# Kernel optimization log

Measured on AMD Instinct MI355X. Metric: run time of the kernel, lower is better.

## Reference

```python
import jax, jax.numpy as jnp
import numpy as np

BETA = 0.25  # commitment loss weight (module default beta=0.25)
K = 1024     # num_of_embeddings


def setup_inputs() -> dict:
    key = jax.random.key(0)
    k1, k2 = jax.random.split(key)
    inputs = jax.random.normal(k1, (16, 256, 64, 64), dtype=jnp.float32)  # NCHW
    codebook = jax.random.normal(k2, (K, 256), dtype=jnp.float32)         # [K, D]
    return {"inputs": inputs, "codebook": codebook}


def reference(inputs, codebook):
    # NCHW -> NHWC, flatten to [N, D]
    x = jnp.transpose(inputs, (0, 2, 3, 1))
    shape_nhwc = x.shape
    flat = x.reshape(-1, codebook.shape[1])  # [N, D]

    dist = (jnp.sum(flat * flat, axis=1, keepdims=True)
            + jnp.sum(codebook * codebook, axis=1)
            - 2.0 * flat @ codebook.T)  # [N, K]
    idx = jnp.argmin(dist, axis=1)  # [N]

    # one-hot @ codebook is just a gather
    zq = codebook[idx].reshape(shape_nhwc)  # [B, H, W, D]

    commitment_loss = jnp.mean((zq - x) ** 2)
    loss = BETA * commitment_loss

    # straight-through estimator
    zq_st = x + jax.lax.stop_gradient(zq - x)

    # perplexity: avg one-hot probs == normalized histogram of code usage
    n = flat.shape[0]
    counts = jnp.zeros((K,), dtype=flat.dtype).at[idx].add(1.0)
    avg_probs = counts / n
    perplexity = jnp.exp(-jnp.sum(avg_probs * jnp.log(avg_probs + 1e-10)))

    z_out = jnp.transpose(zq_st, (0, 3, 1, 2))  # back to NCHW
    return z_out, loss, perplexity, idx[:, None]
```

## Files before the change

### kernel.cpp

```cpp
#include <hip/hip_runtime.h>
#include <math.h>

#define NPTS   65536
#define DDIM   256
#define KCODES 1024
#define HWSZ   4096
#define ZELEMS 16777216
#define CHW    1048576


typedef __attribute__((ext_vector_type(8))) short s16x8;
typedef __attribute__((ext_vector_type(4))) float f32x4;

#define AS1 __attribute__((address_space(1)))
#define AS3 __attribute__((address_space(3)))

__device__ __forceinline__ void bf16split(float x, unsigned short& h, unsigned short& l) {
    unsigned u  = __float_as_uint(x);
    unsigned hu = (u + 0x8000u) & 0xFFFF0000u;
    h = (unsigned short)(hu >> 16);
    float r = x - __uint_as_float(hu);
    l = (unsigned short)((__float_as_uint(r) + 0x8000u) >> 16);
}

__global__ __launch_bounds__(256) void conv_w(const float* __restrict__ cb,
                                              unsigned short* __restrict__ Ws,
                                              float* __restrict__ ww) {
    int gid  = blockIdx.x * 256 + threadIdx.x;
    int code = gid >> 3, o32 = gid & 7;
    int ct = code >> 8, r256 = code & 255, rh = r256 >> 7, rr = r256 & 127;
    unsigned short hi[32], lo[32];
    float ss = 0.f;
#pragma unroll
    for (int j4 = 0; j4 < 8; ++j4) {
        float4 v = *(const float4*)(cb + (size_t)code * DDIM + o32 * 32 + j4 * 4);
        ss += v.x * v.x + v.y * v.y + v.z * v.z + v.w * v.w;
        bf16split(v.x, hi[j4*4+0], lo[j4*4+0]);
        bf16split(v.y, hi[j4*4+1], lo[j4*4+1]);
        bf16split(v.z, hi[j4*4+2], lo[j4*4+2]);
        bf16split(v.w, hi[j4*4+3], lo[j4*4+3]);
    }
    ss += __shfl_down(ss, 4, 8);
    ss += __shfl_down(ss, 2, 8);
    ss += __shfl_down(ss, 1, 8);
    if (o32 == 0) ww[code] = ss;
    size_t bh = (size_t)ct * 131072 + (size_t)o32       * 8192 + rh * 4096 + (rr >> 4) * 512;
    size_t bl = (size_t)ct * 131072 + (size_t)(o32 + 8) * 8192 + rh * 4096 + (rr >> 4) * 512;
#pragma unroll
    for (int oct = 0; oct < 4; ++oct) {
        size_t fo = (size_t)((rr & 15) + 16 * oct) * 8;
        *(s16x8*)(Ws + bh + fo) = *(const s16x8*)&hi[oct * 8];
        *(s16x8*)(Ws + bl + fo) = *(const s16x8*)&lo[oct * 8];
    }
}

__global__ __launch_bounds__(256) void conv_x(const float* __restrict__ in,
                                              unsigned short* __restrict__ Xs,
                                              float* __restrict__ xxpart) {
    __shared__ float xt[32 * 128];
    __shared__ float xps[4];
    const int tid = threadIdx.x;
    const int rg = blockIdx.x >> 3, dc = blockIdx.x & 7;
    const int mt = rg >> 1, rhalf = rg & 1;
    const int b = (rg * 128) >> 12, hw0 = (rg * 128) & 4095;
    const float* src = in + (size_t)b * CHW + (size_t)(dc * 32) * HWSZ + hw0;
    float xs = 0.f;
#pragma unroll
    for (int r = 0; r < 16; ++r) {
        int e = r * 256 + tid, dd = e >> 7, i = e & 127;
        float v = src[(size_t)dd * HWSZ + i];
        xt[dd * 128 + i] = v;
        xs += v * v;
    }
#pragma unroll
    for (int o = 32; o; o >>= 1) xs += __shfl_down(xs, o, 64);
    if ((tid & 63) == 0) xps[tid >> 6] = xs;
    __syncthreads();
    if (tid == 0) xxpart[blockIdx.x] = xps[0] + xps[1] + xps[2] + xps[3];
#pragma unroll
    for (int hl = 0; hl < 2; ++hl) {
        int g = hl * 256 + tid;
        int row = g >> 2, o = g & 3;
        unsigned short hi[8], lo[8];
#pragma unroll
        for (int j = 0; j < 8; ++j)
            bf16split(xt[(o * 8 + j) * 128 + row], hi[j], lo[j]);
        size_t fo = rhalf * 4096 + (size_t)(row >> 4) * 512 + (size_t)((row & 15) + 16 * o) * 8;
        size_t bh = (size_t)mt * 131072 + (size_t)dc       * 8192 + fo;
        size_t bl = (size_t)mt * 131072 + (size_t)(dc + 8) * 8192 + fo;
        *(s16x8*)(Xs + bh) = *(const s16x8*)hi;
        *(s16x8*)(Xs + bl) = *(const s16x8*)lo;
    }
}

__global__ __launch_bounds__(512) void gemm_argmin(
        const unsigned short* __restrict__ Xs, const unsigned short* __restrict__ Ws,
        const float* __restrict__ ww, unsigned long long* __restrict__ pbest) {
    __shared__ unsigned short lds[24576];
    const int tid = threadIdx.x, lane = tid & 63, w = tid >> 6;
    const int wm = w >> 2, wn = w & 3;
    const int col = lane & 15, q = lane >> 4;
    const int bid = blockIdx.x;
    const int xcd = bid & 7, slot = bid >> 3;
    const int nt = slot & 3, mb = (slot >> 2) * 8 + xcd;

    const unsigned short* XsB = Xs + (size_t)mb * 131072;
    const unsigned short* WsB = Ws + (size_t)nt * 131072
                              + (wn >> 1) * 4096 + (wn & 1) * 2048 + lane * 8;

    f32x4 acc[8][4] = {};
    s16x8 B0[4], B1[4];
    const int aoff = wm * 4096 + lane * 8;

    auto SA = [&](int g, int p) {
        const int kA = (g & 7) | ((g >> 4) << 3);
        const unsigned short* s0 = XsB + kA * 8192 + tid * 8;
        __builtin_amdgcn_global_load_lds((const AS1 unsigned*)s0,
            (AS3 unsigned*)&lds[p * 8192 + w * 512], 16, 0, 0);
        __builtin_amdgcn_global_load_lds((const AS1 unsigned*)(s0 + 4096),
            (AS3 unsigned*)&lds[p * 8192 + 4096 + w * 512], 16, 0, 0);
    };
    auto LB = [&](int g, s16x8* B) {
        const int kW = (g & 7) | (((g >> 3) & 1) << 3);
        const s16x8* src = (const s16x8*)(WsB + kW * 8192);
        B[0] = src[0]; B[1] = src[64]; B[2] = src[128]; B[3] = src[192];
    };
#define BAR do { __builtin_amdgcn_s_barrier(); __builtin_amdgcn_sched_barrier(0); } while (0)

    auto TILE = [&](int g, int p, int pstg, const s16x8* Bc, s16x8* Bn, int gate) {
        s16x8 a[8];
#pragma unroll
        for (int mf = 0; mf < 8; ++mf)
            a[mf] = *(const s16x8*)&lds[p * 8192 + aoff + mf * 512];
        if (g + 1 < 24) LB(g + 1, Bn);
        if (g + 2 < 24) SA(g + 2, pstg);
        if (gate == 6)      asm volatile("s_waitcnt vmcnt(6)" ::: "memory");
        else if (gate == 4) asm volatile("s_waitcnt vmcnt(4)" ::: "memory");
        else                asm volatile("s_waitcnt vmcnt(0)" ::: "memory");
        __builtin_amdgcn_sched_barrier(0);
        __builtin_amdgcn_s_setprio(1);
#pragma unroll
        for (int mf = 0; mf < 8; ++mf) {
            acc[mf][0] = __builtin_amdgcn_mfma_f32_16x16x32_bf16(a[mf], Bc[0], acc[mf][0], 0, 0, 0);
            acc[mf][1] = __builtin_amdgcn_mfma_f32_16x16x32_bf16(a[mf], Bc[1], acc[mf][1], 0, 0, 0);
            acc[mf][2] = __builtin_amdgcn_mfma_f32_16x16x32_bf16(a[mf], Bc[2], acc[mf][2], 0, 0, 0);
            acc[mf][3] = __builtin_amdgcn_mfma_f32_16x16x32_bf16(a[mf], Bc[3], acc[mf][3], 0, 0, 0);
        }
        __builtin_amdgcn_s_setprio(0);
        BAR;
    };

    SA(0, 0);
    LB(0, B0);
    SA(1, 1);
    asm volatile("s_waitcnt vmcnt(2)" ::: "memory");
    BAR;

    for (int t6 = 0; t6 < 3; ++t6) {
        TILE(t6 * 6 + 0, 0, 2, B0, B1, 6);
        TILE(t6 * 6 + 1, 1, 0, B1, B0, 6);
        TILE(t6 * 6 + 2, 2, 1, B0, B1, 6);
        TILE(t6 * 6 + 3, 0, 2, B1, B0, 6);
        TILE(t6 * 6 + 4, 1, 0, B0, B1, 6);
        TILE(t6 * 6 + 5, 2, 1, B1, B0, 6);
    }
    TILE(18, 0, 2, B0, B1, 6);
    TILE(19, 1, 0, B1, B0, 6);
    TILE(20, 2, 1, B0, B1, 6);
    TILE(21, 0, 2, B1, B0, 6);
    TILE(22, 1, 0, B0, B1, 4);
    TILE(23, 2, 1, B1, B0, 0);

    __syncthreads();
    unsigned long long* kbuf = (unsigned long long*)lds;
    float wv[4];
#pragma unroll
    for (int nf = 0; nf < 4; ++nf) wv[nf] = ww[nt * 256 + wn * 64 + nf * 16 + col];
#pragma unroll
    for (int mf = 0; mf < 8; ++mf)
#pragma unroll
        for (int r = 0; r < 4; ++r) {
            unsigned long long key = ~0ull;
#pragma unroll
            for (int nf = 0; nf < 4; ++nf) {
                int kg = nt * 256 + wn * 64 + nf * 16 + col;
                float sd = wv[nf] - 2.f * acc[mf][nf][r];
                unsigned u = __float_as_uint(sd);
                u = (u & 0x80000000u) ? ~u : (u | 0x80000000u);
                unsigned long long kk = ((unsigned long long)u << 32) | (unsigned)kg;
                key = kk < key ? kk : key;
            }
#pragma unroll
            for (int off = 1; off < 4; off <<= 1) {
                unsigned klo = __shfl_xor((unsigned)key, off, 64);
                unsigned khi = __shfl_xor((unsigned)(key >> 32), off, 64);
                unsigned long long ok = ((unsigned long long)khi << 32) | klo;
                key = ok < key ? ok : key;
            }
            if ((col & 3) == 0)
                kbuf[(wm * 128 + mf * 16 + q * 4 + r) * 17 + wn * 4 + (col >> 2)] = key;
        }
    __syncthreads();
    if (tid < 256) {
        const unsigned long long* rowp = kbuf + tid * 17;
        unsigned long long km = rowp[0];
#pragma unroll
        for (int i = 1; i < 16; ++i) {
            unsigned long long k = rowp[i];
            km = k < km ? k : km;
        }
        pbest[(size_t)nt * 65536 + mb * 256 + tid] = km;
    }
#undef BAR
}

__global__ __launch_bounds__(256) void gather_kernel(
        const float* __restrict__ cb, const unsigned long long* __restrict__ pbest,
        float* __restrict__ idx_out, unsigned int* __restrict__ counts,
        float* __restrict__ zout, float* __restrict__ partials) {
    const int tid = threadIdx.x;
    const int n   = blockIdx.x * 256 + tid;
    unsigned long long km = pbest[n];
#pragma unroll
    for (int nt = 1; nt < 4; ++nt) {
        unsigned long long k = pbest[(size_t)nt * 65536 + n];
        km = k < km ? k : km;
    }
    const int r = (int)(km & 0xFFFFFFFFu);
    idx_out[n] = (float)r;
    atomicAdd(&counts[r], 1u);

    unsigned m = (unsigned)(km >> 32);
    m = (m & 0x80000000u) ? (m & 0x7FFFFFFFu) : ~m;
    float sd = __uint_as_float(m);

    const int b = n >> 12, hw = n & 4095;
    const float4* row4 = (const float4*)(cb + (size_t)r * DDIM);
    float* zp = zout + (size_t)b * CHW + hw;
#pragma unroll 8
    for (int c4 = 0; c4 < 64; ++c4) {
        float4 v = row4[c4];
        zp[(size_t)(c4 * 4 + 0) * HWSZ] = v.x;
        zp[(size_t)(c4 * 4 + 1) * HWSZ] = v.y;
        zp[(size_t)(c4 * 4 + 2) * HWSZ] = v.z;
        zp[(size_t)(c4 * 4 + 3) * HWSZ] = v.w;
    }
#pragma unroll
    for (int o = 32; o; o >>= 1) sd += __shfl_down(sd, o, 64);
    __shared__ float ps[4];
    if ((tid & 63) == 0) ps[tid >> 6] = sd;
    __syncthreads();
    if (tid == 0) partials[blockIdx.x] = ps[0] + ps[1] + ps[2] + ps[3];
}

__global__ __launch_bounds__(256) void final_kernel(
        const float* __restrict__ partials, const float* __restrict__ xxpart,
        const unsigned int* __restrict__ counts,
        float* __restrict__ out_loss, float* __restrict__ out_perp) {
    const int tid = threadIdx.x;
    float s = partials[tid];
#pragma unroll
    for (int i = 0; i < 16; ++i) s += xxpart[tid * 16 + i];
    float e = 0.f;
#pragma unroll
    for (int qq = 0; qq < 4; ++qq) {
        float p = (float)counts[tid * 4 + qq] * (1.f / 65536.f);
        e += p * logf(p + 1e-10f);
    }
#pragma unroll
    for (int o = 32; o; o >>= 1) {
        s += __shfl_down(s, o, 64);
        e += __shfl_down(e, o, 64);
    }
    __shared__ float ss[4], es[4];
    if ((tid & 63) == 0) { ss[tid >> 6] = s; es[tid >> 6] = e; }
    __syncthreads();
    if (tid == 0) {
        float S = ss[0] + ss[1] + ss[2] + ss[3];
        float E = es[0] + es[1] + es[2] + es[3];
        *out_loss = 0.25f * (S / (float)ZELEMS);
        *out_perp = expf(-E);
    }
}

extern "C" void kernel_launch(void* const* d_in, const int* in_sizes, int n_in,
                              void* d_out, int out_size, void* d_ws, size_t ws_size,
                              hipStream_t stream) {
    (void)in_sizes; (void)n_in; (void)out_size; (void)ws_size;
    const float* in = (const float*)d_in[0];
    const float* cb = (const float*)d_in[1];
    float* out  = (float*)d_out;
    float* zout = out;
    float* loss = out + ZELEMS;
    float* perp = out + ZELEMS + 1;
    float* idxf = out + ZELEMS + 2;

    unsigned int*       counts   = (unsigned int*)d_ws;
    float*              ww       = (float*)((char*)d_ws + 4096);
    float*              partials = (float*)((char*)d_ws + 8192);
    unsigned short*     Ws       = (unsigned short*)((char*)d_ws + 16384);
    unsigned long long* pbest    = (unsigned long long*)((char*)d_ws + 1064960);
    float*              xxpart   = (float*)((char*)d_ws + 3162112);
    unsigned short*     Xs       = (unsigned short*)zout;

    hipMemsetAsync(counts, 0, 4096, stream);
    conv_w      <<<32,   256, 0, stream>>>(cb, Ws, ww);
    conv_x      <<<4096, 256, 0, stream>>>(in, Xs, xxpart);
    gemm_argmin <<<1024, 512, 0, stream>>>(Xs, Ws, ww, pbest);
    gather_kernel<<<256, 256, 0, stream>>>(cb, pbest, idxf, counts, zout, partials);
    final_kernel <<<1,   256, 0, stream>>>(partials, xxpart, counts, loss, perp);
}
```

Baseline: 189.5 us.

## Deepen LDS pipeline to six stages and barrier every other tile

```diff
diff --git a/kernel.cpp b/kernel.cpp
--- a/kernel.cpp
+++ b/kernel.cpp
@@ -96,7 +96,7 @@
 __global__ __launch_bounds__(512) void gemm_argmin(
         const unsigned short* __restrict__ Xs, const unsigned short* __restrict__ Ws,
         const float* __restrict__ ww, unsigned long long* __restrict__ pbest) {
-    __shared__ unsigned short lds[24576];
+    __shared__ unsigned short lds[49152];
     const int tid = threadIdx.x, lane = tid & 63, w = tid >> 6;
     const int wm = w >> 2, wn = w & 3;
     const int col = lane & 15, q = lane >> 4;
@@ -127,13 +127,14 @@
     };
 #define BAR do { __builtin_amdgcn_s_barrier(); __builtin_amdgcn_sched_barrier(0); } while (0)
 
-    auto TILE = [&](int g, int p, int pstg, const s16x8* Bc, s16x8* Bn, int gate) {
+    auto TILE = [&](int g, int p, int pstg, const s16x8* Bc, s16x8* Bn,
+                    int gate, bool dobar) {
         s16x8 a[8];
 #pragma unroll
         for (int mf = 0; mf < 8; ++mf)
             a[mf] = *(const s16x8*)&lds[p * 8192 + aoff + mf * 512];
         if (g + 1 < 24) LB(g + 1, Bn);
-        if (g + 2 < 24) SA(g + 2, pstg);
+        if (g + 4 < 24) SA(g + 4, pstg);
         if (gate == 6)      asm volatile("s_waitcnt vmcnt(6)" ::: "memory");
         else if (gate == 4) asm volatile("s_waitcnt vmcnt(4)" ::: "memory");
         else                asm volatile("s_waitcnt vmcnt(0)" ::: "memory");
@@ -147,29 +148,28 @@
             acc[mf][3] = __builtin_amdgcn_mfma_f32_16x16x32_bf16(a[mf], Bc[3], acc[mf][3], 0, 0, 0);
         }
         __builtin_amdgcn_s_setprio(0);
-        BAR;
+        if (dobar) BAR;
     };
 
-    SA(0, 0);
+    SA(0, 0); SA(1, 1); SA(2, 2); SA(3, 3);
     LB(0, B0);
-    SA(1, 1);
-    asm volatile("s_waitcnt vmcnt(2)" ::: "memory");
+    asm volatile("s_waitcnt vmcnt(4)" ::: "memory");
     BAR;
 
     for (int t6 = 0; t6 < 3; ++t6) {
-        TILE(t6 * 6 + 0, 0, 2, B0, B1, 6);
-        TILE(t6 * 6 + 1, 1, 0, B1, B0, 6);
-        TILE(t6 * 6 + 2, 2, 1, B0, B1, 6);
-        TILE(t6 * 6 + 3, 0, 2, B1, B0, 6);
-        TILE(t6 * 6 + 4, 1, 0, B0, B1, 6);
-        TILE(t6 * 6 + 5, 2, 1, B1, B0, 6);
-    }
-    TILE(18, 0, 2, B0, B1, 6);
-    TILE(19, 1, 0, B1, B0, 6);
-    TILE(20, 2, 1, B0, B1, 6);
-    TILE(21, 0, 2, B1, B0, 6);
-    TILE(22, 1, 0, B0, B1, 4);
-    TILE(23, 2, 1, B1, B0, 0);
+        TILE(t6 * 6 + 0, 0, 4, B0, B1, 6, false);
+        TILE(t6 * 6 + 1, 1, 5, B1, B0, 6, true);
+        TILE(t6 * 6 + 2, 2, 0, B0, B1, 6, false);
+        TILE(t6 * 6 + 3, 3, 1, B1, B0, 6, true);
+        TILE(t6 * 6 + 4, 4, 2, B0, B1, 6, false);
+        TILE(t6 * 6 + 5, 5, 3, B1, B0, 6, true);
+    }
+    TILE(18, 0, 4, B0, B1, 6, false);
+    TILE(19, 1, 5, B1, B0, 6, true);
+    TILE(20, 2, 0, B0, B1, 4, false);
+    TILE(21, 3, 1, B1, B0, 4, true);
+    TILE(22, 4, 2, B0, B1, 4, false);
+    TILE(23, 5, 3, B1, B0, 0, false);
 
     __syncthreads();
     unsigned long long* kbuf = (unsigned long long*)lds;
```

Result: no change. 188.7 us (-0.4%).
